# Optimization experiments

Hardware: AMD Instinct MI355X
Metric: run time of the kernel (lower is better)

Reference implementation:

```python
import math
import jax, jax.numpy as jnp
import numpy as np

IMAGE_SIZE = 256
RADIUS = 10.0  # radius_list=[10.0] default
EYES_POS_LIST = [[-1, -1, -1], [-1, -1, 1], [-1, 1, -1], [-1, 1, 1],
                 [1, -1, -1], [1, -1, 1], [1, 1, -1], [1, 1, 1]]


def _pre_matrix(view_id):
    # projection_matrix @ look_at(eyes, 0, up=(0,0,1)), orthographic branch
    eyes = np.array(EYES_POS_LIST[view_id], np.float32)  # eyepos_scale=1.0
    ups = np.array([0.0, 0.0, 1.0], np.float32)
    z = eyes / max(float(np.linalg.norm(eyes)), 1e-6)
    x = np.cross(ups, z)
    x = x / max(float(np.linalg.norm(x)), 1e-6)
    y = np.cross(z, x)
    orient = np.eye(4, dtype=np.float32)
    orient[0, :3] = x
    orient[1, :3] = y
    orient[2, :3] = z
    trans = np.eye(4, dtype=np.float32)
    trans[:3, 3] = -eyes
    view = orient @ trans
    z_near, z_far = 0.1, 10.0
    proj = np.diag(np.array([1.5, 1.5, -2.0 / (z_far - z_near), 1.0], np.float32))
    proj[2, 3] = (z_far + z_near) / (z_far - z_near)
    return jnp.asarray((proj @ view).astype(np.float32))


def _p2i_max(pos_ij, feat, batch_inds, background, radius):
    """Splat each point onto its (i,j) pixel footprint with a cos kernel,
    reducing with max (background as init). pos_ij in NDC [-1,1]."""
    B, C, H, W = background.shape  # C == 1
    pts = (pos_ij * 0.5 + 0.5) * jnp.array([H - 1.0, W - 1.0], pos_ij.dtype)  # [P,2] pixel coords
    r = int(math.ceil(radius))
    offs = jnp.arange(-r, r + 2)  # cover full footprint around floor(center)
    di, dj = jnp.meshgrid(offs, offs, indexing="ij")
    di = di.reshape(-1)
    dj = dj.reshape(-1)  # [K], K=(2r+2)^2
    base = jnp.floor(pts).astype(jnp.int32)  # [P,2]
    pi = base[:, :1] + di[None, :]  # [P,K]
    pj = base[:, 1:] + dj[None, :]
    d = jnp.sqrt((pi.astype(pts.dtype) - pts[:, :1]) ** 2 +
                 (pj.astype(pts.dtype) - pts[:, 1:]) ** 2)
    w = jnp.where(d <= radius, jnp.cos(d * (jnp.pi / 2.0 / radius)), 0.0)  # cos kernel
    vals = w * feat  # feat [P,1] broadcasts -> [P,K]
    valid = (pi >= 0) & (pi < H) & (pj >= 0) & (pj < W)
    flat = batch_inds[:, None] * (H * W) + pi * W + pj
    flat = jnp.where(valid, flat, B * H * W)  # dump slot for out-of-bounds
    canvas = jnp.full((B * H * W + 1,), -jnp.inf, background.dtype)
    canvas = canvas.at[flat.reshape(-1)].max(vals.reshape(-1))
    return jnp.maximum(background, canvas[:-1].reshape(B, 1, H, W))


def _forward(data, view_id):
    B, N, _ = data.shape
    M = _pre_matrix(view_id)  # [4,4]
    pcd = data.reshape(-1, 3)  # [B*N,3]
    hom = pcd @ M[:, :3].T + M[:, 3][None, :]  # [B*N,4]
    xyz = hom[:, :3] / hom[:, 3:4]
    pos_ij = jnp.stack([-xyz[:, 1], xyz[:, 0]], axis=1)  # (i,j) = (-y, x)
    z = xyz[:, 2:3]
    feat = 1.0 - (z - z.min()) / (z.max() - z.min())  # [B*N,1]
    batch_inds = jnp.repeat(jnp.arange(B, dtype=jnp.int32), N)
    background = jnp.zeros((B, 1, IMAGE_SIZE, IMAGE_SIZE), data.dtype)
    return _p2i_max(pos_ij, feat, batch_inds, background, RADIUS)


def setup_inputs() -> dict:
    key = jax.random.key(0)
    data = jax.random.normal(key, (32, 4096, 3), dtype=jnp.float32) * 0.5  # unit-ish cloud
    return {"data": data, "view_id": 0}


def reference(data, view_id):
    return _forward(data, view_id)
```

## Files before the change

kernel.cpp:

```cpp
#include <hip/hip_runtime.h>
#include <math.h>

#define IMG_H 256
#define IMG_W 256
#define NBATCH 32
#define NPER 4096
#define NPTS (NBATCH * NPER)
#define STRIP 8
#define NSTRIPS (IMG_H / STRIP)
#define THREADS 512
#define NWAVES (THREADS / 64)
#define PADL 19
#define ROWW 299
#define CANVAS_W (STRIP * ROWW)
#define KC  0.15707964f
#define KC3 0.47123890f
#define TMAX 2.4674011f
#define BBLK 512
#define WPB 16
#define WCAP 256
#define SCH 512


struct Mats { float m[8][12]; };

static void build_mats(float out[8][12]) {
  static const double EYES[8][3] = {
    {-1,-1,-1},{-1,-1, 1},{-1, 1,-1},{-1, 1, 1},
    { 1,-1,-1},{ 1,-1, 1},{ 1, 1,-1},{ 1, 1, 1}};
  for (int v = 0; v < 8; ++v) {
    const double* e = EYES[v];
    double en = sqrt(e[0]*e[0] + e[1]*e[1] + e[2]*e[2]);
    if (en < 1e-6) en = 1e-6;
    double z[3] = {e[0]/en, e[1]/en, e[2]/en};
    double x[3] = {-z[1], z[0], 0.0};
    double xn = sqrt(x[0]*x[0] + x[1]*x[1]);
    if (xn < 1e-6) xn = 1e-6;
    x[0] /= xn; x[1] /= xn; x[2] = 0.0;
    double y[3] = {z[1]*x[2] - z[2]*x[1],
                   z[2]*x[0] - z[0]*x[2],
                   z[0]*x[1] - z[1]*x[0]};
    const double s  = 1.5;
    const double pz = -2.0 / (10.0 - 0.1);
    const double c3 = (10.0 + 0.1) / (10.0 - 0.1);
    double dxe = x[0]*e[0] + x[1]*e[1] + x[2]*e[2];
    double dye = y[0]*e[0] + y[1]*e[1] + y[2]*e[2];
    double dze = z[0]*e[0] + z[1]*e[1] + z[2]*e[2];
    out[v][0] = (float)(s*x[0]); out[v][1] = (float)(s*x[1]);
    out[v][2] = (float)(s*x[2]); out[v][3] = (float)(-s*dxe);
    out[v][4] = (float)(s*y[0]); out[v][5] = (float)(s*y[1]);
    out[v][6] = (float)(s*y[2]); out[v][7] = (float)(-s*dye);
    out[v][8] = (float)(pz*z[0]); out[v][9] = (float)(pz*z[1]);
    out[v][10] = (float)(pz*z[2]); out[v][11] = (float)(-pz*dze + c3);
  }
}

__global__ __launch_bounds__(256)
void bin_agg(const float* __restrict__ data,
             const int* __restrict__ view_id,
             Mats mats, unsigned int* __restrict__ counts,
             float4* __restrict__ rec, float* __restrict__ red) {
  __shared__ unsigned int hist[NSTRIPS];
  __shared__ float smn[4], smx[4];

  const int tid  = threadIdx.x;
  const int blk  = blockIdx.x;
  const int b    = blk >> 4;
  const int kblk = blk & 15;
  const int p    = blk * 256 + tid;

  if (tid < NSTRIPS) hist[tid] = 0u;
  __syncthreads();

  const int v = (*view_id) & 7;
  const float* M = mats.m[v];
  float x = data[3*p+0], y = data[3*p+1], zz = data[3*p+2];
  float h1 = M[4]*x + M[5]*y + M[6]*zz + M[7];
  float pif = (-h1 * 0.5f + 0.5f) * (float)(IMG_H - 1);
  int base_i = (int)floorf(pif);
  int lo = max(base_i - 9, 0), hi = min(base_i + 10, IMG_H - 1);
  float h0 = M[0]*x + M[1]*y + M[2]*zz + M[3];
  float pjf = (h0 * 0.5f + 0.5f) * (float)(IMG_W - 1);
  int base_j = (int)floorf(pjf);
  float h2 = M[8]*x + M[9]*y + M[10]*zz + M[11];

  bool valid = (lo <= hi) & (base_j >= -10) & (base_j <= IMG_W + 8);
  int s0 = lo >> 3, s1 = valid ? (hi >> 3) : (lo >> 3) - 1;

  unsigned fr0 = 0xFFFFFFFFu, fr1 = 0xFFFFFFFFu,
           fr2 = 0xFFFFFFFFu, fr3 = 0xFFFFFFFFu;
  if (valid) {
    fr0 = atomicAdd(&hist[s0], 1u) | ((unsigned)s0 << 16);
    if (s0 + 1 <= s1) fr1 = atomicAdd(&hist[s0 + 1], 1u) | ((unsigned)(s0 + 1) << 16);
    if (s0 + 2 <= s1) fr2 = atomicAdd(&hist[s0 + 2], 1u) | ((unsigned)(s0 + 2) << 16);
    if (s0 + 3 <= s1) fr3 = atomicAdd(&hist[s0 + 3], 1u) | ((unsigned)(s0 + 3) << 16);
  }

  float zmn = h2, zmx = h2;
#pragma unroll
  for (int m = 32; m >= 1; m >>= 1) {
    zmn = fminf(zmn, __shfl_xor(zmn, m, 64));
    zmx = fmaxf(zmx, __shfl_xor(zmx, m, 64));
  }
  if ((tid & 63) == 0) { smn[tid >> 6] = zmn; smx[tid >> 6] = zmx; }

  __syncthreads();

  if (tid < NSTRIPS) counts[blk * NSTRIPS + tid] = hist[tid];
  if (tid == 64) {
    red[blk] = fminf(fminf(smn[0], smn[1]), fminf(smn[2], smn[3]));
    red[BBLK + blk] = fmaxf(fmaxf(smx[0], smx[1]), fmaxf(smx[2], smx[3]));
  }

  if (valid) {
    float fj_s = ((float)(base_j - 9) - pjf) * KC;
#pragma unroll
    for (int k = 0; k < 4; ++k) {
      unsigned fr = (k == 0) ? fr0 : (k == 1) ? fr1 : (k == 2) ? fr2 : fr3;
      if (fr != 0xFFFFFFFFu) {
        int s = (int)(fr >> 16);
        unsigned idx = fr & 0xFFFFu;
        int i0 = max(lo, s * STRIP);
        int i1 = min(hi, s * STRIP + (STRIP - 1));
        int rows = i1 - i0 + 1;
        int basew = (i0 - s * STRIP) * ROWW + (base_j + 10);
        unsigned meta = ((unsigned)rows << 12) | (unsigned)basew;
        float fi_s = ((float)i0 - pif) * KC;
        rec[((size_t)(b * NSTRIPS + s) * WPB + kblk) * WCAP + idx] =
            make_float4(fi_s, fj_s, h2, __uint_as_float(meta));
      }
    }
  }
}

__global__ __launch_bounds__(THREADS, 8)
void splat_drain(const unsigned int* __restrict__ counts,
                 const float4* __restrict__ rec,
                 const float* __restrict__ red,
                 float* __restrict__ out) {
  __shared__ unsigned int canvas[CANVAS_W];
  __shared__ float4 stage[SCH];
  __shared__ int off[WPB + 1];
  __shared__ int c16[WPB];
  __shared__ float zred[2];

  const int tid  = threadIdx.x;
  const int lane = tid & 63;
  const int wid  = tid >> 6;
  const int b    = blockIdx.y;
  const int strip = (blockIdx.x + b) & 31;
  const int bin  = b * NSTRIPS + strip;

  for (int i = tid; i < CANVAS_W; i += THREADS) canvas[i] = 0u;

  if (tid < 64) {
    float a = INFINITY, c = -INFINITY;
#pragma unroll
    for (int k = 0; k < BBLK / 64; ++k) {
      a = fminf(a, red[tid + 64 * k]);
      c = fmaxf(c, red[BBLK + tid + 64 * k]);
    }
#pragma unroll
    for (int m = 32; m >= 1; m >>= 1) {
      a = fminf(a, __shfl_xor(a, m, 64));
      c = fmaxf(c, __shfl_xor(c, m, 64));
    }
    if (tid == 0) { zred[0] = a; zred[1] = c; }
  } else if (tid >= 64 && tid < 80) {
    int k = tid - 64;
    int c = (int)counts[(b * WPB + k) * NSTRIPS + strip];
    int s = c;
#pragma unroll
    for (int d = 1; d < 16; d <<= 1) {
      int y2 = __shfl_up(s, d, 64);
      if (k >= d) s += y2;
    }
    off[k] = s - c;
    c16[k] = c;
    if (k == 15) off[16] = s;
  }
  __syncthreads();

  const float zmin = zred[0];
  const float zinv = 1.0f / (zred[1] - zmin);
  const int n = off[16];

  const int r_l   = (lane * 3277) >> 16;
  const int col_l = lane - r_l * 20;
  const float col_kc = (float)col_l * KC;
  const float r_kc   = (float)r_l * KC;

  const int g16 = tid >> 5;
  const int l32 = tid & 31;
  const float4* win = rec + ((size_t)bin * WPB + g16) * WCAP;
  const int wlo = off[g16];
  const int whi = wlo + c16[g16];

  for (int c0 = 0; c0 < n; c0 += SCH) {
    const int cend = min(c0 + SCH, n);
    if (c0) __syncthreads();
    {
      int lo = max(wlo, c0), hi2 = min(whi, cend);
      for (int g = lo + l32; g < hi2; g += 32)
        stage[g - c0] = win[g - wlo];
    }
    __syncthreads();

    const int m = cend - c0;
    if (lane < 60) {
      for (int e = wid; e < m; e += NWAVES) {
        float4 Q = stage[e];
        float fi_s = Q.x, fj_s = Q.y;
        unsigned meta = __float_as_uint(Q.w);
        float feat = fmaxf(1.0f - (Q.z - zmin) * zinv, 0.0f);
        int basew = (int)(meta & 0xFFFu);
        int rows  = (int)(meta >> 12);
        float dy = col_kc + fj_s;
        float dy2 = dy * dy;
        float dx = r_kc + fi_s;
        unsigned int* ptr = canvas + (basew + r_l * ROWW + col_l);
        int rb = 0;
        for (; rb + 3 <= rows; rb += 3) {
          float t = fminf(__builtin_fmaf(dx, dx, dy2), TMAX);
          float w = __builtin_fmaf(t,
                      __builtin_fmaf(t,
                        __builtin_fmaf(t,
                          __builtin_fmaf(t, 2.4801587e-5f, -1.3888889e-3f),
                          4.1666668e-2f),
                        -0.5f),
                      1.0f);
          atomicMax(ptr, __float_as_uint(w * feat));
          dx += KC3;
          ptr += 3 * ROWW;
        }
        if (rb < rows) {
          int row = min(rb + r_l, rows - 1);
          float dxt = __builtin_fmaf((float)row, KC, fi_s);
          float t = fminf(__builtin_fmaf(dxt, dxt, dy2), TMAX);
          float w = __builtin_fmaf(t,
                      __builtin_fmaf(t,
                        __builtin_fmaf(t,
                          __builtin_fmaf(t, 2.4801587e-5f, -1.3888889e-3f),
                          4.1666668e-2f),
                        -0.5f),
                      1.0f);
          atomicMax(canvas + (basew + row * ROWW + col_l),
                    __float_as_uint(w * feat));
        }
      }
    }
  }

  __syncthreads();
  float* outb = out + ((size_t)b * IMG_H + strip * STRIP) * IMG_W;
#pragma unroll
  for (int i = tid; i < STRIP * IMG_W; i += THREADS) {
    int r = i >> 8, col = i & 255;
    outb[i] = __uint_as_float(canvas[r * ROWW + PADL + col]);
  }
}

extern "C" void kernel_launch(void* const* d_in, const int* in_sizes, int n_in,
                              void* d_out, int out_size, void* d_ws, size_t ws_size,
                              hipStream_t stream) {
  const float* data = (const float*)d_in[0];
  const int* view_id = (const int*)d_in[1];
  float* out = (float*)d_out;

  unsigned int* counts = (unsigned int*)d_ws;
  float* red = (float*)((char*)d_ws + 65536);
  float4* rec = (float4*)((char*)d_ws + 131072);

  Mats mats;
  build_mats(mats.m);

  bin_agg<<<BBLK, 256, 0, stream>>>(data, view_id, mats, counts, rec, red);
  dim3 grid(NSTRIPS, NBATCH);
  splat_drain<<<grid, THREADS, 0, stream>>>(counts, rec, red, out);
}
```

Before: 33.72 us.

## Double strip height to 16 rows and use 1024-thread splat blocks

```diff
diff --git a/kernel.cpp b/kernel.cpp
--- a/kernel.cpp
+++ b/kernel.cpp
@@ -6,9 +6,9 @@
 #define NBATCH 32
 #define NPER 4096
 #define NPTS (NBATCH * NPER)
-#define STRIP 8
+#define STRIP 16
 #define NSTRIPS (IMG_H / STRIP)
-#define THREADS 512
+#define THREADS 1024
 #define NWAVES (THREADS / 64)
 #define PADL 19
 #define ROWW 299
@@ -19,7 +19,7 @@
 #define BBLK 512
 #define WPB 16
 #define WCAP 256
-#define SCH 512
+#define SCH 1024
 
 
 struct Mats { float m[8][12]; };
@@ -60,16 +60,18 @@
              const int* __restrict__ view_id,
              Mats mats, unsigned int* __restrict__ counts,
              float4* __restrict__ rec, float* __restrict__ red) {
-  __shared__ unsigned int hist[NSTRIPS];
+  __shared__ unsigned int hist[4][17];
+  __shared__ unsigned int wbase[4][17];
   __shared__ float smn[4], smx[4];
 
   const int tid  = threadIdx.x;
+  const int w    = tid >> 6;
   const int blk  = blockIdx.x;
   const int b    = blk >> 4;
   const int kblk = blk & 15;
   const int p    = blk * 256 + tid;
 
-  if (tid < NSTRIPS) hist[tid] = 0u;
+  if (tid < 68) ((unsigned int*)hist)[tid] = 0u;
   __syncthreads();
 
   const int v = (*view_id) & 7;
@@ -85,15 +87,13 @@
   float h2 = M[8]*x + M[9]*y + M[10]*zz + M[11];
 
   bool valid = (lo <= hi) & (base_j >= -10) & (base_j <= IMG_W + 8);
-  int s0 = lo >> 3, s1 = valid ? (hi >> 3) : (lo >> 3) - 1;
-
-  unsigned fr0 = 0xFFFFFFFFu, fr1 = 0xFFFFFFFFu,
-           fr2 = 0xFFFFFFFFu, fr3 = 0xFFFFFFFFu;
+  int s0 = lo >> 4, s1 = valid ? (hi >> 4) : (lo >> 4) - 1;
+
+  unsigned fr0 = 0xFFFFFFFFu, fr1 = 0xFFFFFFFFu, fr2 = 0xFFFFFFFFu;
   if (valid) {
-    fr0 = atomicAdd(&hist[s0], 1u) | ((unsigned)s0 << 16);
-    if (s0 + 1 <= s1) fr1 = atomicAdd(&hist[s0 + 1], 1u) | ((unsigned)(s0 + 1) << 16);
-    if (s0 + 2 <= s1) fr2 = atomicAdd(&hist[s0 + 2], 1u) | ((unsigned)(s0 + 2) << 16);
-    if (s0 + 3 <= s1) fr3 = atomicAdd(&hist[s0 + 3], 1u) | ((unsigned)(s0 + 3) << 16);
+    fr0 = atomicAdd(&hist[w][s0], 1u) | ((unsigned)s0 << 16);
+    if (s0 + 1 <= s1) fr1 = atomicAdd(&hist[w][s0 + 1], 1u) | ((unsigned)(s0 + 1) << 16);
+    if (s0 + 2 <= s1) fr2 = atomicAdd(&hist[w][s0 + 2], 1u) | ((unsigned)(s0 + 2) << 16);
   }
 
   float zmn = h2, zmx = h2;
@@ -102,29 +102,41 @@
     zmn = fminf(zmn, __shfl_xor(zmn, m, 64));
     zmx = fmaxf(zmx, __shfl_xor(zmx, m, 64));
   }
-  if ((tid & 63) == 0) { smn[tid >> 6] = zmn; smx[tid >> 6] = zmx; }
-
-  __syncthreads();
-
-  if (tid < NSTRIPS) counts[blk * NSTRIPS + tid] = hist[tid];
+  if ((tid & 63) == 0) { smn[w] = zmn; smx[w] = zmx; }
+
+  __syncthreads();
+
+  if (tid < 64) {
+    int s = tid >> 2, ww = tid & 3;
+    unsigned val = hist[ww][s];
+    unsigned acc = val;
+#pragma unroll
+    for (int d = 1; d < 4; d <<= 1) {
+      unsigned t = __shfl_up(acc, d, 64);
+      if (ww >= d) acc += t;
+    }
+    wbase[ww][s] = acc - val;
+    if (ww == 3) counts[blk * NSTRIPS + s] = acc;
+  }
   if (tid == 64) {
     red[blk] = fminf(fminf(smn[0], smn[1]), fminf(smn[2], smn[3]));
     red[BBLK + blk] = fmaxf(fmaxf(smx[0], smx[1]), fmaxf(smx[2], smx[3]));
   }
+  __syncthreads();
 
   if (valid) {
     float fj_s = ((float)(base_j - 9) - pjf) * KC;
 #pragma unroll
-    for (int k = 0; k < 4; ++k) {
-      unsigned fr = (k == 0) ? fr0 : (k == 1) ? fr1 : (k == 2) ? fr2 : fr3;
+    for (int k = 0; k < 3; ++k) {
+      unsigned fr = (k == 0) ? fr0 : (k == 1) ? fr1 : fr2;
       if (fr != 0xFFFFFFFFu) {
         int s = (int)(fr >> 16);
-        unsigned idx = fr & 0xFFFFu;
+        unsigned idx = wbase[w][s] + (fr & 0xFFFFu);
         int i0 = max(lo, s * STRIP);
         int i1 = min(hi, s * STRIP + (STRIP - 1));
         int rows = i1 - i0 + 1;
         int basew = (i0 - s * STRIP) * ROWW + (base_j + 10);
-        unsigned meta = ((unsigned)rows << 12) | (unsigned)basew;
+        unsigned meta = ((unsigned)rows << 13) | (unsigned)basew;
         float fi_s = ((float)i0 - pif) * KC;
         rec[((size_t)(b * NSTRIPS + s) * WPB + kblk) * WCAP + idx] =
             make_float4(fi_s, fj_s, h2, __uint_as_float(meta));
@@ -148,7 +160,7 @@
   const int lane = tid & 63;
   const int wid  = tid >> 6;
   const int b    = blockIdx.y;
-  const int strip = (blockIdx.x + b) & 31;
+  const int strip = (blockIdx.x * 7 + b) & 15;
   const int bin  = b * NSTRIPS + strip;
 
   for (int i = tid; i < CANVAS_W; i += THREADS) canvas[i] = 0u;
@@ -190,8 +202,8 @@
   const float col_kc = (float)col_l * KC;
   const float r_kc   = (float)r_l * KC;
 
-  const int g16 = tid >> 5;
-  const int l32 = tid & 31;
+  const int g16 = tid >> 6;
+  const int l64 = tid & 63;
   const float4* win = rec + ((size_t)bin * WPB + g16) * WCAP;
   const int wlo = off[g16];
   const int whi = wlo + c16[g16];
@@ -201,7 +213,7 @@
     if (c0) __syncthreads();
     {
       int lo = max(wlo, c0), hi2 = min(whi, cend);
-      for (int g = lo + l32; g < hi2; g += 32)
+      for (int g = lo + l64; g < hi2; g += 64)
         stage[g - c0] = win[g - wlo];
     }
     __syncthreads();
@@ -213,8 +225,8 @@
         float fi_s = Q.x, fj_s = Q.y;
         unsigned meta = __float_as_uint(Q.w);
         float feat = fmaxf(1.0f - (Q.z - zmin) * zinv, 0.0f);
-        int basew = (int)(meta & 0xFFFu);
-        int rows  = (int)(meta >> 12);
+        int basew = (int)(meta & 0x1FFFu);
+        int rows  = (int)(meta >> 13);
         float dy = col_kc + fj_s;
         float dy2 = dy * dy;
         float dx = r_kc + fi_s;
```

Measured after the change: 33.20 us (median of 2 runs). About the same (-1.5%).
